# Performance work log

Measured on AMD Instinct MI355X. Metric: run time of the kernel, lower is better.

Reference implementation:

```python
import jax, jax.numpy as jnp
import numpy as np

LAMBD = 0.05

def _mlp(y, W0, b0, W1, b1, W2, b2, W3, b3):
    h = jax.nn.relu(y @ W0.T + b0)
    h = jax.nn.relu(h @ W1.T + b1)
    h = jax.nn.relu(h @ W2.T + b2)
    return h @ W3.T + b3  # [N, 1]


def setup_inputs() -> dict:
    key = jax.random.key(0)
    ks = jax.random.split(key, 8)
    B, N, D = 4096, 20000, 784
    s = lambda fan_in: 1.0 / np.sqrt(fan_in)
    return {
        "x": jax.random.normal(ks[0], (B, D), jnp.float32),
        "y": jax.random.normal(ks[1], (N, D), jnp.float32),
        "nu": jax.random.uniform(ks[2], (N,), jnp.float32, 0.1, 1.0),
        "W0": jax.random.normal(ks[3], (512, D), jnp.float32) * s(D),
        "b0": jnp.zeros((512,), jnp.float32),
        "W1": jax.random.normal(ks[4], (256, 512), jnp.float32) * s(512),
        "b1": jnp.zeros((256,), jnp.float32),
        "W2": jax.random.normal(ks[5], (128, 256), jnp.float32) * s(256),
        "b2": jnp.zeros((128,), jnp.float32),
        "W3": jax.random.normal(ks[6], (1, 128), jnp.float32) * s(128),
        "b3": jnp.zeros((1,), jnp.float32),
    }


def reference(x, y, nu, W0, b0, W1, b1, W2, b2, W3, b3):
    # squared-distance cost matrix [B, N], normalized by mean(|y|^2)
    sy2 = jnp.sum(y * y, axis=1)            # [N]
    normalization = sy2.mean()
    cxy = (jnp.sum(x * x, axis=1, keepdims=True) + sy2[None, :]
           - 2.0 * (x @ y.T)) / normalization  # [B, N]
    psiy = _mlp(y, W0, b0, W1, b1, W2, b2, W3, b3)[:, 0]  # [N]
    # entropic semi-dual: -lambd * logsumexp((psi(y) - c(x,y))/lambd + log nu)
    z = (psiy[None, :] - cxy) / LAMBD + jnp.log(nu)[None, :]
    out = -LAMBD * jax.nn.logsumexp(z, axis=1) + psiy.mean()  # [B]
    return out
```

## Files before the change

### kernel.cpp

```cpp
#include <hip/hip_runtime.h>
#include <math.h>
#include <stdint.h>
#include <stddef.h>

#define B_ROWS 4096
#define N_REAL 20000
#define NP2    20224
#define NJT2   79
#define NRT    16
#define D_IN   784
#define DP2    800
#define NKS    25
#define NKT    13
#define YBLK   316
#define XBLK   64
#define PW     158
#define LAMBD  0.05f
#define LN2    0.69314718055994530942f
#define QS     (4.5f / 127.f)
#define QINV   (127.f / 4.5f)

typedef __attribute__((ext_vector_type(8))) short bf16x8;
typedef __attribute__((ext_vector_type(4))) float f32x4;
typedef __attribute__((ext_vector_type(4))) int   i32x4;

typedef const unsigned int __attribute__((address_space(1)))* gas_u32p;
typedef unsigned int __attribute__((address_space(3)))* las_u32p;

static __device__ __forceinline__ void gload_lds16(const void* g, void* l) {
  __builtin_amdgcn_global_load_lds((gas_u32p)g, (las_u32p)l, 16, 0, 0);
}

static __device__ __forceinline__ float bf2f(short s) {
  union { unsigned u; float f; } c;
  c.u = ((unsigned)(unsigned short)s) << 16;
  return c.f;
}
static __device__ __forceinline__ short f2bf(float f) {
  union { float f; unsigned u; } c;
  c.f = f;
  unsigned r = (c.u + 0x7fffu + ((c.u >> 16) & 1u)) >> 16;
  return (short)(unsigned short)r;
}
static __device__ __forceinline__ unsigned q4c(float a, float b, float c, float d) {
  int x0 = min(127, max(-127, (int)rintf(a * QINV))) & 255;
  int x1 = min(127, max(-127, (int)rintf(b * QINV))) & 255;
  int x2 = min(127, max(-127, (int)rintf(c * QINV))) & 255;
  int x3 = min(127, max(-127, (int)rintf(d * QINV))) & 255;
  return (unsigned)(x0 | (x1 << 8) | (x2 << 16) | (x3 << 24));
}

__global__ void k_prep(const float* __restrict__ ysrc, const float* __restrict__ xsrc,
                       unsigned char* __restrict__ y_i8, unsigned char* __restrict__ x_i8,
                       short* __restrict__ y_bf, float* __restrict__ sy2,
                       float* __restrict__ x2,
                       const float* __restrict__ W0, const float* __restrict__ W1,
                       const float* __restrict__ W2, short* __restrict__ W0b,
                       short* __restrict__ W1b, short* __restrict__ W2b,
                       unsigned* __restrict__ ctr) {
  const int b = blockIdx.x, t = threadIdx.x;
  if (b == 0 && t == 0) *ctr = 0u;

  if (b >= YBLK + XBLK) {
    const int wb_ = b - (YBLK + XBLK);
    const float* src; short* dst; int r, cs, cp;
    if (wb_ < 512)      { r = wb_;       src = W0; dst = W0b; cs = D_IN; cp = DP2; }
    else if (wb_ < 768) { r = wb_ - 512; src = W1; dst = W1b; cs = 512;  cp = 512; }
    else                { r = wb_ - 768; src = W2; dst = W2b; cs = 256;  cp = 256; }
    const float* sp = src + (size_t)r * cs;
    short* dp = dst + (size_t)r * cp;
    for (int c = t; c < cp; c += 256)
      dp[c] = f2bf(c < cs ? sp[c] : 0.f);
    return;
  }

  const float* src; unsigned char* di8; float* rowsum;
  int rows_real, g; bool wbf;
  if (b < YBLK) { src = ysrc; di8 = y_i8; rowsum = sy2;
                  rows_real = N_REAL; g = b; wbf = true; }
  else          { src = xsrc; di8 = x_i8; rowsum = x2;
                  rows_real = B_ROWS; g = b - YBLK; wbf = false; }
  const int q = t & 3, r = t >> 2;
  const int grow = g * 64 + r;
  const int tile1 = grow >> 8, sub1 = grow & 255;
  const float* sp = src + (size_t)grow * D_IN;
  const bool realRow = grow < rows_real;
  float sq = 0.f;

  for (int kt = 0; kt < NKT; ++kt) {
    const int c0 = kt * 64 + q * 16;
    float v[16];
    if (realRow && c0 < D_IN) {
      #pragma unroll
      for (int u = 0; u < 4; ++u) {
        float4 w4 = *(const float4*)(sp + c0 + u * 4);
        v[u*4+0] = w4.x; v[u*4+1] = w4.y; v[u*4+2] = w4.z; v[u*4+3] = w4.w;
        sq += w4.x * w4.x + w4.y * w4.y + w4.z * w4.z + w4.w * w4.w;
      }
    } else {
      #pragma unroll
      for (int e = 0; e < 16; ++e) v[e] = 0.f;
    }
    uint4 pk;
    pk.x = q4c(v[0],  v[1],  v[2],  v[3]);
    pk.y = q4c(v[4],  v[5],  v[6],  v[7]);
    pk.z = q4c(v[8],  v[9],  v[10], v[11]);
    pk.w = q4c(v[12], v[13], v[14], v[15]);
    *(uint4*)(di8 + (size_t)(tile1 * NKT + kt) * 16384
              + ((size_t)(q * 256 + sub1) << 4)) = pk;
    if (wbf) {
      const int ks = kt * 2 + (q >> 1);
      if (ks < NKS) {
        const int oct = (q & 1) * 2;
        short* dp = y_bf + (size_t)(tile1 * NKS + ks) * 8192
                  + ((size_t)(oct * 256 + sub1) << 3);
        bf16x8 o0, o1;
        #pragma unroll
        for (int e = 0; e < 8; ++e) { o0[e] = f2bf(v[e]); o1[e] = f2bf(v[8 + e]); }
        *(bf16x8*)dp = o0;
        *(bf16x8*)(dp + 2048) = o1;
      }
    }
  }

  sq += __shfl_xor(sq, 1, 4);
  sq += __shfl_xor(sq, 2, 4);
  if (q == 0 && realRow) rowsum[grow] = sq;
}

template <bool TA>
__global__ __launch_bounds__(256) void k_gemmf(const short* __restrict__ A,
                                               const short* __restrict__ Bm,
                                               const float* __restrict__ bias,
                                               short* __restrict__ C,
                                               int K, int Ncols,
                                               const float* __restrict__ W3c,
                                               const float* __restrict__ b3c,
                                               float* __restrict__ psiOut,
                                               const float* __restrict__ sy2n,
                                               float* __restrict__ scaln) {
  extern __shared__ short L[];
  __shared__ float pbuf[256];
  const int t = threadIdx.x;
  const int rb = blockIdx.y, cb = blockIdx.x;

  if (sy2n != nullptr && rb == NP2 / 128) {
    if (cb != 0) return;
    __shared__ float red[4];
    float a = 0.f;
    for (int j = t; j < N_REAL; j += 256) a += sy2n[j];
    #pragma unroll
    for (int m = 1; m < 64; m <<= 1) a += __shfl_xor(a, m, 64);
    if ((t & 63) == 0) red[t >> 6] = a;
    __syncthreads();
    if (t == 0) {
      float norm = (red[0] + red[1] + red[2] + red[3]) / (float)N_REAL;
      scaln[0] = norm;
      scaln[1] = 1.0f / norm;
      scaln[2] = 2.0f / (norm * LAMBD * LN2);
    }
    return;
  }

  const int lane = t & 63, wave = t >> 6;
  const int lr = lane & 15, lg = lane >> 4;
  const int wrow = (wave >> 1) * 64, wcol = (wave & 1) * 64;
  const int KS = K >> 5;
  const int wb = wave * 512;

  const int prow = t & 127, psel = t >> 7;
  const short* aS0; const short* aS1; int aStep;
  if constexpr (TA) {
    const short* base = A + (size_t)((rb >> 1) * NKS) * 8192
                      + ((size_t)((rb & 1) * 128 + prow) << 3);
    aS0 = base + (size_t)(psel * 2048);
    aS1 = base + (size_t)((2 + psel) * 2048);
    aStep = 8192;
  } else {
    const short* base = A + (size_t)(rb * 128 + prow) * K;
    aS0 = base + psel * 8;
    aS1 = base + (2 + psel) * 8;
    aStep = 32;
  }
  const short* bBase = Bm + (size_t)(cb * 128 + prow) * K;
  const short* bS0 = bBase + psel * 8;
  const short* bS1 = bBase + (2 + psel) * 8;

  auto stage = [&](int s) {
    short* Lb = L + (s % 3) * 8192;
    gload_lds16(aS0 + (size_t)s * aStep, Lb + wb);
    gload_lds16(aS1 + (size_t)s * aStep, Lb + 2048 + wb);
    gload_lds16(bS0 + (size_t)s * 32,    Lb + 4096 + wb);
    gload_lds16(bS1 + (size_t)s * 32,    Lb + 4096 + 2048 + wb);
  };

  f32x4 acc[4][4];
  #pragma unroll
  for (int mi = 0; mi < 4; ++mi)
    #pragma unroll
    for (int ni = 0; ni < 4; ++ni)
      acc[mi][ni] = (f32x4){0.f, 0.f, 0.f, 0.f};

  stage(0);
  stage(1);
  asm volatile("s_waitcnt vmcnt(4)" ::: "memory");
  __builtin_amdgcn_s_barrier();
  __builtin_amdgcn_sched_barrier(0);

  const int aro = (wrow + lr) * 8;
  const int bro = (wcol + lr) * 8;
  for (int ks = 0; ks < KS; ++ks) {
    if (ks + 2 < KS) stage(ks + 2);
    const short* LA = L + (ks % 3) * 8192 + lg * 1024;
    const short* LB = LA + 4096;
    bf16x8 b0 = *(const bf16x8*)&LB[bro];
    bf16x8 b1 = *(const bf16x8*)&LB[bro + 128];
    bf16x8 b2 = *(const bf16x8*)&LB[bro + 256];
    bf16x8 b3 = *(const bf16x8*)&LB[bro + 384];
    bf16x8 a0 = *(const bf16x8*)&LA[aro];
    bf16x8 a1 = *(const bf16x8*)&LA[aro + 128];
    bf16x8 a2v = *(const bf16x8*)&LA[aro + 256];
    bf16x8 a3v = *(const bf16x8*)&LA[aro + 384];
    __builtin_amdgcn_s_setprio(1);
    #pragma unroll
    for (int ni = 0; ni < 4; ++ni) {
      bf16x8 bv = ni == 0 ? b0 : ni == 1 ? b1 : ni == 2 ? b2 : b3;
      acc[0][ni] = __builtin_amdgcn_mfma_f32_16x16x32_bf16(a0, bv, acc[0][ni], 0, 0, 0);
      acc[1][ni] = __builtin_amdgcn_mfma_f32_16x16x32_bf16(a1, bv, acc[1][ni], 0, 0, 0);
      acc[2][ni] = __builtin_amdgcn_mfma_f32_16x16x32_bf16(a2v, bv, acc[2][ni], 0, 0, 0);
      acc[3][ni] = __builtin_amdgcn_mfma_f32_16x16x32_bf16(a3v, bv, acc[3][ni], 0, 0, 0);
    }
    __builtin_amdgcn_s_setprio(0);
    if (ks + 2 < KS) {
      asm volatile("s_waitcnt vmcnt(4)" ::: "memory");
      __builtin_amdgcn_s_barrier();
      __builtin_amdgcn_sched_barrier(0);
    } else if (ks + 1 < KS) {
      asm volatile("s_waitcnt vmcnt(0)" ::: "memory");
      __builtin_amdgcn_s_barrier();
      __builtin_amdgcn_sched_barrier(0);
    }
  }

  if (psiOut == nullptr) {
    #pragma unroll
    for (int ni = 0; ni < 4; ++ni) {
      const int col = cb * 128 + wcol + ni * 16 + lr;
      const float bv = bias[col];
      #pragma unroll
      for (int mi = 0; mi < 4; ++mi) {
        const int row0 = rb * 128 + wrow + mi * 16 + lg * 4;
        #pragma unroll
        for (int r = 0; r < 4; ++r)
          C[(size_t)(row0 + r) * Ncols + col] = f2bf(fmaxf(acc[mi][ni][r] + bv, 0.f));
      }
    }
  } else {
    float part[4][4];
    #pragma unroll
    for (int mi = 0; mi < 4; ++mi)
      #pragma unroll
      for (int r = 0; r < 4; ++r) part[mi][r] = 0.f;
    #pragma unroll
    for (int ni = 0; ni < 4; ++ni) {
      const int col = wcol + ni * 16 + lr;
      const float bv = bias[col];
      const float w3 = W3c[col];
      #pragma unroll
      for (int mi = 0; mi < 4; ++mi)
        #pragma unroll
        for (int r = 0; r < 4; ++r)
          part[mi][r] += fmaxf(acc[mi][ni][r] + bv, 0.f) * w3;
    }
    #pragma unroll
    for (int mi = 0; mi < 4; ++mi)
      #pragma unroll
      for (int r = 0; r < 4; ++r) {
        float s = part[mi][r];
        s += __shfl_xor(s, 1, 16);
        s += __shfl_xor(s, 2, 16);
        s += __shfl_xor(s, 4, 16);
        s += __shfl_xor(s, 8, 16);
        part[mi][r] = s;
      }
    if (lr == 0) {
      #pragma unroll
      for (int mi = 0; mi < 4; ++mi)
        #pragma unroll
        for (int r = 0; r < 4; ++r)
          pbuf[(wave & 1) * 128 + (wave >> 1) * 64 + mi * 16 + lg * 4 + r] = part[mi][r];
    }
    __syncthreads();
    if (t < 128) psiOut[rb * 128 + t] = pbuf[t] + pbuf[t + 128] + b3c[0];
  }
}

__global__ void k_a2(const float* __restrict__ psi, const float* __restrict__ sy2,
                     const float* __restrict__ nu, const float* __restrict__ scal,
                     float* __restrict__ a2raw, float* __restrict__ maxp,
                     float* __restrict__ sump, unsigned* __restrict__ ctr,
                     float* __restrict__ scalw) {
  const int j = blockIdx.x * 256 + threadIdx.x;
  const float invn = scal[1];
  float a = -1e30f, p = 0.f;
  if (j < NP2) {
    if (j < N_REAL) {
      p = psi[j];
      a = (p - sy2[j] * invn) * (1.0f / (LAMBD * LN2)) + log2f(nu[j]);
    }
    a2raw[j] = a;
  }
  __shared__ float redm[4], reds[4];
  __shared__ int lastFlag;
  #pragma unroll
  for (int m = 1; m < 64; m <<= 1) {
    a = fmaxf(a, __shfl_xor(a, m, 64));
    p += __shfl_xor(p, m, 64);
  }
  const int t = threadIdx.x;
  if ((t & 63) == 0) { redm[t >> 6] = a; reds[t >> 6] = p; }
  __syncthreads();
  if (t == 0) {
    maxp[blockIdx.x] = fmaxf(fmaxf(redm[0], redm[1]), fmaxf(redm[2], redm[3]));
    sump[blockIdx.x] = reds[0] + reds[1] + reds[2] + reds[3];
    __threadfence();
    lastFlag = (atomicAdd(ctr, 1u) == (unsigned)(gridDim.x - 1));
  }
  __syncthreads();
  if (lastFlag) {
    __threadfence();
    float am = -1e30f, s = 0.f;
    for (int i = t; i < (int)gridDim.x; i += 256) {
      am = fmaxf(am, maxp[i]);
      s += sump[i];
    }
    #pragma unroll
    for (int m = 1; m < 64; m <<= 1) {
      am = fmaxf(am, __shfl_xor(am, m, 64));
      s += __shfl_xor(s, m, 64);
    }
    if ((t & 63) == 0) { redm[t >> 6] = am; reds[t >> 6] = s; }
    __syncthreads();
    if (t == 0) {
      scalw[3] = fmaxf(fmaxf(redm[0], redm[1]), fmaxf(redm[2], redm[3]));
      scalw[4] = (reds[0] + reds[1] + reds[2] + reds[3]) / (float)N_REAL;
    }
  }
}

__global__ __launch_bounds__(512, 2) void k_flash(const unsigned char* __restrict__ x_t,
                                                  const unsigned char* __restrict__ y_t,
                                                  const float* __restrict__ a2raw,
                                                  const float* __restrict__ scal,
                                                  float* __restrict__ parts) {
  extern __shared__ char Lsh[];
  const int t = threadIdx.x;
  const int lane = t & 63, wave = t >> 6;
  const int lr = lane & 15, lg = lane >> 4;
  const int wr = wave >> 1, wc = wave & 1;
  const int rbt = blockIdx.x, jt = blockIdx.y;

  const float s2c1 = QS * QS * scal[2];
  const float A2 = scal[3];

  const int t16 = t * 16;
  const int wb = wave * 1024;
  const int aoff = (lg * 256 + wr * 64 + lr) * 16;
  const int boff = (lg * 256 + wc * 128 + lr) * 16;

  const unsigned char* As = x_t + (size_t)(rbt * NKT) * 16384 + t16;
  const unsigned char* Bs = y_t + (size_t)(jt * NKT) * 16384 + t16;

  i32x4 acc[4][8];
  #pragma unroll
  for (int mi = 0; mi < 4; ++mi)
    #pragma unroll
    for (int ni = 0; ni < 8; ++ni)
      acc[mi][ni] = (i32x4){0, 0, 0, 0};

  auto stage = [&](int s) {
    char* Lb = Lsh + (s % 3) * 32768;
    const unsigned char* An = As + (size_t)s * 16384;
    const unsigned char* Bn = Bs + (size_t)s * 16384;
    gload_lds16(An,         Lb + wb);
    gload_lds16(An + 8192,  Lb + 8192 + wb);
    gload_lds16(Bn,         Lb + 16384 + wb);
    gload_lds16(Bn + 8192,  Lb + 24576 + wb);
  };

  stage(0);
  stage(1);
  asm volatile("s_waitcnt vmcnt(4)" ::: "memory");
  __builtin_amdgcn_s_barrier();
  __builtin_amdgcn_sched_barrier(0);

  #pragma unroll
  for (int ks = 0; ks < NKT; ++ks) {
    if (ks + 2 < NKT) stage(ks + 2);
    const char* LA = Lsh + (ks % 3) * 32768;
    const char* LB = LA + 16384;
    i32x4 bf[8];
    #pragma unroll
    for (int ni = 0; ni < 8; ++ni)
      bf[ni] = *(const i32x4*)(LB + boff + ni * 256);
    i32x4 af[4];
    #pragma unroll
    for (int mi = 0; mi < 4; ++mi)
      af[mi] = *(const i32x4*)(LA + aoff + mi * 256);
    __builtin_amdgcn_s_setprio(1);
    #pragma unroll
    for (int ni = 0; ni < 8; ++ni) {
      acc[0][ni] = __builtin_amdgcn_mfma_i32_16x16x64_i8(af[0], bf[ni], acc[0][ni], 0, 0, 0);
      acc[1][ni] = __builtin_amdgcn_mfma_i32_16x16x64_i8(af[1], bf[ni], acc[1][ni], 0, 0, 0);
      acc[2][ni] = __builtin_amdgcn_mfma_i32_16x16x64_i8(af[2], bf[ni], acc[2][ni], 0, 0, 0);
      acc[3][ni] = __builtin_amdgcn_mfma_i32_16x16x64_i8(af[3], bf[ni], acc[3][ni], 0, 0, 0);
    }
    __builtin_amdgcn_s_setprio(0);
    if (ks + 2 < NKT) {
      asm volatile("s_waitcnt vmcnt(4)" ::: "memory");
      __builtin_amdgcn_s_barrier();
      __builtin_amdgcn_sched_barrier(0);
    } else if (ks + 1 < NKT) {
      asm volatile("s_waitcnt vmcnt(0)" ::: "memory");
      __builtin_amdgcn_s_barrier();
      __builtin_amdgcn_sched_barrier(0);
    }
  }

  const int colb = jt * 256 + wc * 128 + lr;
  float av[8];
  #pragma unroll
  for (int ni = 0; ni < 8; ++ni)
    av[ni] = a2raw[colb + ni * 16] - A2;
  #pragma unroll
  for (int mi = 0; mi < 4; ++mi)
    #pragma unroll
    for (int r = 0; r < 4; ++r) {
      const int row = rbt * 256 + wr * 64 + mi * 16 + lg * 4 + r;
      float s = 0.f;
      #pragma unroll
      for (int ni = 0; ni < 8; ++ni)
        s += exp2f((float)acc[mi][ni][r] * s2c1 + av[ni]);
      s += __shfl_xor(s, 1, 16);
      s += __shfl_xor(s, 2, 16);
      s += __shfl_xor(s, 4, 16);
      s += __shfl_xor(s, 8, 16);
      if (lr == 0)
        parts[(size_t)row * PW + jt * 2 + wc] = s;
    }
}

__global__ void k_comb(const float* __restrict__ parts, const float* __restrict__ x2,
                       const float* __restrict__ scal, float* __restrict__ out) {
  const int wave = threadIdx.x >> 6, lane = threadIdx.x & 63;
  const int row = blockIdx.x * 4 + wave;
  const float* pr = parts + (size_t)row * PW;
  float s = 0.f;
  for (int i = lane; i < PW; i += 64) s += pr[i];
  #pragma unroll
  for (int m = 1; m < 64; m <<= 1) s += __shfl_xor(s, m, 64);
  if (lane == 0)
    out[row] = -(LAMBD * LN2) * (scal[3] + log2f(s)) + x2[row] * scal[1] + scal[4];
}

extern "C" void kernel_launch(void* const* d_in, const int* in_sizes, int n_in,
                              void* d_out, int out_size, void* d_ws, size_t ws_size,
                              hipStream_t stream) {
  const float* x  = (const float*)d_in[0];
  const float* y  = (const float*)d_in[1];
  const float* nu = (const float*)d_in[2];
  const float* W0 = (const float*)d_in[3];
  const float* b0 = (const float*)d_in[4];
  const float* W1 = (const float*)d_in[5];
  const float* b1 = (const float*)d_in[6];
  const float* W2 = (const float*)d_in[7];
  const float* b2 = (const float*)d_in[8];
  const float* W3 = (const float*)d_in[9];
  const float* b3 = (const float*)d_in[10];
  float* out = (float*)d_out;

  char* w = (char*)d_ws;
  auto alloc = [&](size_t bytes) {
    char* p = w;
    w += (bytes + 255) & ~(size_t)255;
    return p;
  };
  unsigned char* y_i8 = (unsigned char*)alloc((size_t)NJT2 * NKT * 16384);
  unsigned char* x_i8 = (unsigned char*)alloc((size_t)NRT * NKT * 16384);
  short* y_bf  = (short*)alloc((size_t)(NP2 / 256) * NKS * 8192 * 2);
  short* W0b   = (short*)alloc((size_t)512 * DP2 * 2);
  short* W1b   = (short*)alloc((size_t)256 * 512 * 2);
  short* W2b   = (short*)alloc((size_t)128 * 256 * 2);
  short* H1    = (short*)alloc((size_t)NP2 * 512 * 2);
  short* H2    = (short*)alloc((size_t)NP2 * 256 * 2);
  float* sy2   = (float*)alloc((size_t)N_REAL * 4);
  float* x2    = (float*)alloc((size_t)B_ROWS * 4);
  float* psi   = (float*)alloc((size_t)NP2 * 4);
  float* a2raw = (float*)alloc((size_t)NP2 * 4);
  float* maxp  = (float*)alloc(128 * 4);
  float* sump  = (float*)alloc(128 * 4);
  float* scal  = (float*)alloc(64 * 4);
  unsigned* ctr = (unsigned*)alloc(256);
  float* parts = (float*)alloc((size_t)B_ROWS * PW * 4);

  k_prep<<<dim3(YBLK + XBLK + 896), dim3(256), 0, stream>>>(y, x, y_i8, x_i8, y_bf,
                                                            sy2, x2, W0, W1, W2,
                                                            W0b, W1b, W2b, ctr);

  hipFuncSetAttribute((const void*)k_gemmf<true>, hipFuncAttributeMaxDynamicSharedMemorySize, 49152);
  hipFuncSetAttribute((const void*)k_gemmf<false>, hipFuncAttributeMaxDynamicSharedMemorySize, 49152);
  k_gemmf<true><<<dim3(4, NP2 / 128 + 1), dim3(256), 49152, stream>>>(
      y_bf, W0b, b0, H1, DP2, 512, nullptr, nullptr, nullptr, sy2, scal);
  k_gemmf<false><<<dim3(2, NP2 / 128), dim3(256), 49152, stream>>>(
      H1, W1b, b1, H2, 512, 256, nullptr, nullptr, nullptr, nullptr, nullptr);
  k_gemmf<false><<<dim3(1, NP2 / 128), dim3(256), 49152, stream>>>(
      H2, W2b, b2, nullptr, 256, 128, W3, b3, psi, nullptr, nullptr);

  k_a2<<<dim3(NP2 / 256), dim3(256), 0, stream>>>(psi, sy2, nu, scal, a2raw,
                                                  maxp, sump, ctr, scal);

  hipFuncSetAttribute((const void*)k_flash, hipFuncAttributeMaxDynamicSharedMemorySize, 98304);
  k_flash<<<dim3(NRT, NJT2), dim3(512), 98304, stream>>>(x_i8, y_i8, a2raw, scal, parts);
  k_comb<<<dim3(B_ROWS / 4), dim3(256), 0, stream>>>(parts, x2, scal, out);
}
```

Before: 186.5 us.

## Fuse MLP layers 2 and 3 into one kernel keeping H2 in LDS

Replaces two separate GEMM launches (H1·W1 → H2 in global memory, then H2·W2 with W3 reduction) with a single kernel per 128-row block. Each block computes the full 256-wide layer-2 output, writes it bf16 into LDS in MFMA-friendly layout, loads W2 into LDS, and then runs layer 3 plus the W3 dot-product reduction. This removes the H2 global round trip and one launch. In exchange each block uses 136 KB of LDS and more accumulator registers, which lowers occupancy, and the grid is only 158 blocks.

Result: faster. 173.5 us, median of 2 (-7.0%).

```diff
diff --git a/kernel.cpp b/kernel.cpp
--- a/kernel.cpp
+++ b/kernel.cpp
@@ -134,13 +134,9 @@
                                                const float* __restrict__ bias,
                                                short* __restrict__ C,
                                                int K, int Ncols,
-                                               const float* __restrict__ W3c,
-                                               const float* __restrict__ b3c,
-                                               float* __restrict__ psiOut,
                                                const float* __restrict__ sy2n,
                                                float* __restrict__ scaln) {
   extern __shared__ short L[];
-  __shared__ float pbuf[256];
   const int t = threadIdx.x;
   const int rb = blockIdx.y, cb = blockIdx.x;
 
@@ -242,57 +238,194 @@
     }
   }
 
-  if (psiOut == nullptr) {
-    #pragma unroll
-    for (int ni = 0; ni < 4; ++ni) {
-      const int col = cb * 128 + wcol + ni * 16 + lr;
-      const float bv = bias[col];
-      #pragma unroll
-      for (int mi = 0; mi < 4; ++mi) {
-        const int row0 = rb * 128 + wrow + mi * 16 + lg * 4;
-        #pragma unroll
-        for (int r = 0; r < 4; ++r)
-          C[(size_t)(row0 + r) * Ncols + col] = f2bf(fmaxf(acc[mi][ni][r] + bv, 0.f));
+  #pragma unroll
+  for (int ni = 0; ni < 4; ++ni) {
+    const int col = cb * 128 + wcol + ni * 16 + lr;
+    const float bv = bias[col];
+    #pragma unroll
+    for (int mi = 0; mi < 4; ++mi) {
+      const int row0 = rb * 128 + wrow + mi * 16 + lg * 4;
+      #pragma unroll
+      for (int r = 0; r < 4; ++r)
+        C[(size_t)(row0 + r) * Ncols + col] = f2bf(fmaxf(acc[mi][ni][r] + bv, 0.f));
+    }
+  }
+}
+
+__global__ __launch_bounds__(256) void k_mlp12(const short* __restrict__ H1,
+                                               const short* __restrict__ W1b,
+                                               const float* __restrict__ b1,
+                                               const short* __restrict__ W2b,
+                                               const float* __restrict__ b2,
+                                               const float* __restrict__ W3,
+                                               const float* __restrict__ b3,
+                                               float* __restrict__ psi) {
+  extern __shared__ short L[];
+  const int t = threadIdx.x;
+  const int lane = t & 63, wave = t >> 6;
+  const int lr = lane & 15, lg = lane >> 4;
+  const int wr = wave >> 1, wc2 = wave & 1;
+  const int rb = blockIdx.x;
+  const int wb = wave * 512;
+
+  float b1v[8], b2v[4], w3v[4];
+  #pragma unroll
+  for (int ni = 0; ni < 8; ++ni) b1v[ni] = b1[wc2 * 128 + ni * 16 + lr];
+  #pragma unroll
+  for (int ni = 0; ni < 4; ++ni) {
+    b2v[ni] = b2[wc2 * 64 + ni * 16 + lr];
+    w3v[ni] = W3[wc2 * 64 + ni * 16 + lr];
+  }
+  const float b3v = b3[0];
+
+  const int prow = t & 127, psel = t >> 7;
+  const short* aBase = H1 + (size_t)(rb * 128 + prow) * 512;
+  const short* aS0 = aBase + psel * 8;
+  const short* aS1 = aBase + (2 + psel) * 8;
+  const int bcol = wave * 64 + lane;
+  const short* bBase = W1b + (size_t)bcol * 512;
+
+  auto stageA = [&](int s) {
+    short* Lb = L + (s % 3) * 12288;
+    gload_lds16(aS0 + s * 32, Lb + wb);
+    gload_lds16(aS1 + s * 32, Lb + 2048 + wb);
+    #pragma unroll
+    for (int j = 0; j < 4; ++j)
+      gload_lds16(bBase + s * 32 + j * 8, Lb + 4096 + j * 2048 + wb);
+  };
+
+  f32x4 acc[4][8];
+  #pragma unroll
+  for (int mi = 0; mi < 4; ++mi)
+    #pragma unroll
+    for (int ni = 0; ni < 8; ++ni)
+      acc[mi][ni] = (f32x4){0.f, 0.f, 0.f, 0.f};
+
+  stageA(0);
+  stageA(1);
+  asm volatile("s_waitcnt vmcnt(6)" ::: "memory");
+  __builtin_amdgcn_s_barrier();
+  __builtin_amdgcn_sched_barrier(0);
+
+  const int aro = (wr * 64 + lr) * 8;
+  const int bro = (wc2 * 128 + lr) * 8;
+  for (int ks = 0; ks < 16; ++ks) {
+    if (ks + 2 < 16) stageA(ks + 2);
+    const short* LA = L + (ks % 3) * 12288 + lg * 1024;
+    const short* LB = L + (ks % 3) * 12288 + 4096 + lg * 2048;
+    bf16x8 af[4];
+    #pragma unroll
+    for (int mi = 0; mi < 4; ++mi)
+      af[mi] = *(const bf16x8*)&LA[aro + mi * 128];
+    bf16x8 bfr[8];
+    #pragma unroll
+    for (int ni = 0; ni < 8; ++ni)
+      bfr[ni] = *(const bf16x8*)&LB[bro + ni * 128];
+    __builtin_amdgcn_s_setprio(1);
+    #pragma unroll
+    for (int ni = 0; ni < 8; ++ni) {
+      acc[0][ni] = __builtin_amdgcn_mfma_f32_16x16x32_bf16(af[0], bfr[ni], acc[0][ni], 0, 0, 0);
+      acc[1][ni] = __builtin_amdgcn_mfma_f32_16x16x32_bf16(af[1], bfr[ni], acc[1][ni], 0, 0, 0);
+      acc[2][ni] = __builtin_amdgcn_mfma_f32_16x16x32_bf16(af[2], bfr[ni], acc[2][ni], 0, 0, 0);
+      acc[3][ni] = __builtin_amdgcn_mfma_f32_16x16x32_bf16(af[3], bfr[ni], acc[3][ni], 0, 0, 0);
+    }
+    __builtin_amdgcn_s_setprio(0);
+    if (ks + 2 < 16) {
+      asm volatile("s_waitcnt vmcnt(6)" ::: "memory");
+      __builtin_amdgcn_s_barrier();
+      __builtin_amdgcn_sched_barrier(0);
+    } else if (ks + 1 < 16) {
+      asm volatile("s_waitcnt vmcnt(0)" ::: "memory");
+      __builtin_amdgcn_s_barrier();
+      __builtin_amdgcn_sched_barrier(0);
+    }
+  }
+  __syncthreads();
+
+  #pragma unroll
+  for (int j = 0; j < 16; ++j) {
+    const int bbyte = j * 4096 + wave * 1024 + lane * 16;
+    const int ks2 = bbyte >> 13, kc = (bbyte >> 11) & 3, row = (bbyte >> 4) & 127;
+    gload_lds16(W2b + row * 256 + ks2 * 32 + kc * 8, L + j * 2048 + wb);
+  }
+
+  short* H2i = L + 36864;
+  #pragma unroll
+  for (int ni = 0; ni < 8; ++ni) {
+    const int col = wc2 * 128 + ni * 16 + lr;
+    const int ks2 = col >> 5, kc = (col >> 3) & 3, e = col & 7;
+    const float bv = b1v[ni];
+    #pragma unroll
+    for (int mi = 0; mi < 4; ++mi)
+      #pragma unroll
+      for (int r = 0; r < 4; ++r) {
+        const int row = wr * 64 + mi * 16 + lg * 4 + r;
+        H2i[ks2 * 4096 + kc * 1024 + row * 8 + e] =
+            f2bf(fmaxf(acc[mi][ni][r] + bv, 0.f));
       }
-    }
-  } else {
-    float part[4][4];
+  }
+  asm volatile("s_waitcnt vmcnt(0)" ::: "memory");
+  __syncthreads();
+
+  f32x4 acc2[4][4];
+  #pragma unroll
+  for (int mi = 0; mi < 4; ++mi)
+    #pragma unroll
+    for (int ni = 0; ni < 4; ++ni)
+      acc2[mi][ni] = (f32x4){0.f, 0.f, 0.f, 0.f};
+  const int aro2 = (wr * 64 + lr) * 8;
+  const int bro2 = (wc2 * 64 + lr) * 8;
+  #pragma unroll
+  for (int ks = 0; ks < 8; ++ks) {
+    const short* HA = H2i + ks * 4096 + lg * 1024;
+    const short* WB = L + ks * 4096 + lg * 1024;
+    bf16x8 af[4], bfr[4];
+    #pragma unroll
+    for (int mi = 0; mi < 4; ++mi) af[mi] = *(const bf16x8*)&HA[aro2 + mi * 128];
+    #pragma unroll
+    for (int ni = 0; ni < 4; ++ni) bfr[ni] = *(const bf16x8*)&WB[bro2 + ni * 128];
     #pragma unroll
     for (int mi = 0; mi < 4; ++mi)
       #pragma unroll
-      for (int r = 0; r < 4; ++r) part[mi][r] = 0.f;
-    #pragma unroll
-    for (int ni = 0; ni < 4; ++ni) {
-      const int col = wcol + ni * 16 + lr;
-      const float bv = bias[col];
-      const float w3 = W3c[col];
-      #pragma unroll
-      for (int mi = 0; mi < 4; ++mi)
-        #pragma unroll
-        for (int r = 0; r < 4; ++r)
-          part[mi][r] += fmaxf(acc[mi][ni][r] + bv, 0.f) * w3;
-    }
+      for (int ni = 0; ni < 4; ++ni)
+        acc2[mi][ni] = __builtin_amdgcn_mfma_f32_16x16x32_bf16(af[mi], bfr[ni], acc2[mi][ni], 0, 0, 0);
+  }
+
+  float part[4][4];
+  #pragma unroll
+  for (int mi = 0; mi < 4; ++mi)
+    #pragma unroll
+    for (int r = 0; r < 4; ++r) part[mi][r] = 0.f;
+  #pragma unroll
+  for (int ni = 0; ni < 4; ++ni) {
     #pragma unroll
     for (int mi = 0; mi < 4; ++mi)
       #pragma unroll
-      for (int r = 0; r < 4; ++r) {
-        float s = part[mi][r];
-        s += __shfl_xor(s, 1, 16);
-        s += __shfl_xor(s, 2, 16);
-        s += __shfl_xor(s, 4, 16);
-        s += __shfl_xor(s, 8, 16);
-        part[mi][r] = s;
-      }
-    if (lr == 0) {
-      #pragma unroll
-      for (int mi = 0; mi < 4; ++mi)
-        #pragma unroll
-        for (int r = 0; r < 4; ++r)
-          pbuf[(wave & 1) * 128 + (wave >> 1) * 64 + mi * 16 + lg * 4 + r] = part[mi][r];
-    }
-    __syncthreads();
-    if (t < 128) psiOut[rb * 128 + t] = pbuf[t] + pbuf[t + 128] + b3c[0];
-  }
+      for (int r = 0; r < 4; ++r)
+        part[mi][r] += fmaxf(acc2[mi][ni][r] + b2v[ni], 0.f) * w3v[ni];
+  }
+  #pragma unroll
+  for (int mi = 0; mi < 4; ++mi)
+    #pragma unroll
+    for (int r = 0; r < 4; ++r) {
+      float s = part[mi][r];
+      s += __shfl_xor(s, 1, 16);
+      s += __shfl_xor(s, 2, 16);
+      s += __shfl_xor(s, 4, 16);
+      s += __shfl_xor(s, 8, 16);
+      part[mi][r] = s;
+    }
+  __syncthreads();
+  float* pbuf = (float*)L;
+  if (lr == 0) {
+    #pragma unroll
+    for (int mi = 0; mi < 4; ++mi)
+      #pragma unroll
+      for (int r = 0; r < 4; ++r)
+        pbuf[wc2 * 128 + wr * 64 + mi * 16 + lg * 4 + r] = part[mi][r];
+  }
+  __syncthreads();
+  if (t < 128) psi[rb * 128 + t] = pbuf[t] + pbuf[t + 128] + b3v;
 }
 
 __global__ void k_a2(const float* __restrict__ psi, const float* __restrict__ sy2,
@@ -492,7 +625,6 @@
   short* W1b   = (short*)alloc((size_t)256 * 512 * 2);
   short* W2b   = (short*)alloc((size_t)128 * 256 * 2);
   short* H1    = (short*)alloc((size_t)NP2 * 512 * 2);
-  short* H2    = (short*)alloc((size_t)NP2 * 256 * 2);
   float* sy2   = (float*)alloc((size_t)N_REAL * 4);
   float* x2    = (float*)alloc((size_t)B_ROWS * 4);
   float* psi   = (float*)alloc((size_t)NP2 * 4);
@@ -508,13 +640,11 @@
                                                             W0b, W1b, W2b, ctr);
 
   hipFuncSetAttribute((const void*)k_gemmf<true>, hipFuncAttributeMaxDynamicSharedMemorySize, 49152);
-  hipFuncSetAttribute((const void*)k_gemmf<false>, hipFuncAttributeMaxDynamicSharedMemorySize, 49152);
   k_gemmf<true><<<dim3(4, NP2 / 128 + 1), dim3(256), 49152, stream>>>(
-      y_bf, W0b, b0, H1, DP2, 512, nullptr, nullptr, nullptr, sy2, scal);
-  k_gemmf<false><<<dim3(2, NP2 / 128), dim3(256), 49152, stream>>>(
-      H1, W1b, b1, H2, 512, 256, nullptr, nullptr, nullptr, nullptr, nullptr);
-  k_gemmf<false><<<dim3(1, NP2 / 128), dim3(256), 49152, stream>>>(
-      H2, W2b, b2, nullptr, 256, 128, W3, b3, psi, nullptr, nullptr);
+      y_bf, W0b, b0, H1, DP2, 512, sy2, scal);
+
+  hipFuncSetAttribute((const void*)k_mlp12, hipFuncAttributeMaxDynamicSharedMemorySize, 139264);
+  k_mlp12<<<dim3(NP2 / 128), dim3(256), 139264, stream>>>(H1, W1b, b1, W2b, b2, W3, b3, psi);
 
   k_a2<<<dim3(NP2 / 256), dim3(256), 0, stream>>>(psi, sy2, nu, scal, a2raw,
                                                   maxp, sump, ctr, scal);
```
